# Optimization experiments

Hardware: AMD Instinct MI355X
Metric: run time of the kernel (lower is better)

Reference implementation:

```python
import jax, jax.numpy as jnp
import numpy as np

IN_FEATURES = 4096
OUT_FEATURES = 4096
CLUSTERING_FRAC = 0.1
IC = int(IN_FEATURES * CLUSTERING_FRAC)  # 409 clustering synapses
HILL_N = 2.0
HILL_KD = 0.5 ** 2  # k_a ** n
BATCH = 8192


def setup_inputs() -> dict:
    key = jax.random.key(0)
    k1, k2, k3, k4 = jax.random.split(key, 4)
    x = jax.random.normal(k1, (BATCH, IN_FEATURES), dtype=jnp.float32)
    # Linear default init scale ~ 1/sqrt(fan_in)
    W_nmda = jax.random.normal(k2, (OUT_FEATURES, IC), dtype=jnp.float32) / np.sqrt(IC)
    W_non = jax.random.normal(k3, (OUT_FEATURES, IN_FEATURES - IC), dtype=jnp.float32) / np.sqrt(IN_FEATURES - IC)
    b_non = jax.random.normal(k4, (OUT_FEATURES,), dtype=jnp.float32) / np.sqrt(IN_FEATURES - IC)
    return {"x": x, "W_nmda": W_nmda, "W_non": W_non, "b_non": b_non}


def reference(x, W_nmda, W_non, b_non):
    # Split synapses into clustering (nmda) and non-clustering groups.
    x_c = x[:, :IC]          # [B, 409]
    x_nc = x[:, IC:]         # [B, 3687]

    # state = sigmoid(non_nmda(x_nc)) - 1  (<= 0)
    state = jax.nn.sigmoid(x_nc @ W_non.T + b_non) - 1.0  # [B, O]

    # conv1d(kernel=[1,1], stride=1) over per-synapse products then sum over
    # window positions == weighted sum with coeff 2 for interior, 1 at edges.
    coeff = jnp.full((IC,), 2.0, dtype=x.dtype).at[0].set(1.0).at[-1].set(1.0)
    cluster_activity = (x_c * coeff) @ W_nmda.T  # [B, O]

    pre = cluster_activity + state
    # Hill(n=2, k_a=0.5): x^n / (k_d + x^n)
    xn = pre ** HILL_N
    return xn / (HILL_KD + xn)
```

## Files before the change

### kernel.cpp

```cpp
#include <hip/hip_runtime.h>
#include <hip/hip_bf16.h>
#include <cstdint>
#include <cstddef>

typedef unsigned short u16;
typedef __bf16 bf16x8 __attribute__((ext_vector_type(8)));
typedef float f32x4 __attribute__((ext_vector_type(4)));
typedef float f32x4u __attribute__((ext_vector_type(4), aligned(4)));

#define IN_F   4096
#define OUT_F  4096
#define IC_N   409
#define K_NON  3687
#define K_HI0  3712
#define K_LO0  4121
#define K_HI1  4530
#define K_END  4939
#define K_TOT  4992
#define BATCHN 8192
#define NT     78
#define T_SPLIT 58

__device__ __forceinline__ u16 f2bf(float f) {
  uint32_t u = __float_as_uint(f);
  uint32_t r = (u + 0x7FFFu + ((u >> 16) & 1u)) >> 16;
  return (u16)r;
}
__device__ __forceinline__ float bf2f(u16 h) {
  return __uint_as_float(((uint32_t)h) << 16);
}
__device__ __forceinline__ float coefj(int j) {
  return (j == 0 || j == IC_N - 1) ? 1.0f : 2.0f;
}

__global__ __launch_bounds__(256) void pack_a_kernel(const float* __restrict__ x,
                                                     u16* __restrict__ Ab) {
  __shared__ u16 hbuf[IC_N];
  __shared__ u16 lbuf[IC_N];
  const int row = blockIdx.x;
  const float* xr = x + (size_t)row * IN_F;
  for (int j = threadIdx.x; j < IC_N; j += 256) {
    const float v = xr[j] * coefj(j);
    const u16 h = f2bf(v);
    hbuf[j] = h;
    lbuf[j] = f2bf(v - bf2f(h));
  }
  __syncthreads();
  u16* outr = Ab + (size_t)row * K_TOT;
  for (int c8 = threadIdx.x; c8 < K_TOT / 8; c8 += 256) {
    const int kb = c8 * 8;
    u16 tmp[8] __attribute__((aligned(16)));
    if (kb + 8 <= K_NON) {
      const float* s = xr + IC_N + kb;
      const f32x4u v0 = *(const f32x4u*)s;
      const f32x4u v1 = *(const f32x4u*)(s + 4);
#pragma unroll
      for (int e = 0; e < 4; ++e) { tmp[e] = f2bf(v0[e]); tmp[4 + e] = f2bf(v1[e]); }
    } else if (kb < K_HI0) {
#pragma unroll
      for (int e = 0; e < 8; ++e) {
        const int k = kb + e;
        tmp[e] = (k < K_NON) ? f2bf(xr[IC_N + k]) : (u16)0;
      }
    } else {
#pragma unroll
      for (int e = 0; e < 8; ++e) {
        const int k = kb + e;
        u16 o;
        if (k < K_LO0)      o = hbuf[k - K_HI0];
        else if (k < K_HI1) o = lbuf[k - K_LO0];
        else if (k < K_END) o = hbuf[k - K_HI1];
        else                o = 0;
        tmp[e] = o;
      }
    }
    *(int4*)(outr + kb) = *(const int4*)tmp;
  }
}

__global__ __launch_bounds__(256) void pack_b_kernel(const float* __restrict__ Wnon,
                                                     const float* __restrict__ Wnmda,
                                                     u16* __restrict__ Bb) {
  __shared__ u16 hbuf[IC_N];
  __shared__ u16 lbuf[IC_N];
  const int row = blockIdx.x;
  const float* wr = Wnon + (size_t)row * K_NON;
  const float* wc = Wnmda + (size_t)row * IC_N;
  for (int j = threadIdx.x; j < IC_N; j += 256) {
    const float v = wc[j];
    const u16 h = f2bf(v);
    hbuf[j] = h;
    lbuf[j] = f2bf(v - bf2f(h));
  }
  __syncthreads();
  u16* outr = Bb + (size_t)row * K_TOT;
  for (int c8 = threadIdx.x; c8 < K_TOT / 8; c8 += 256) {
    const int kb = c8 * 8;
    u16 tmp[8] __attribute__((aligned(16)));
    if (kb + 8 <= K_NON) {
      const float* s = wr + kb;
      const f32x4u v0 = *(const f32x4u*)s;
      const f32x4u v1 = *(const f32x4u*)(s + 4);
#pragma unroll
      for (int e = 0; e < 4; ++e) { tmp[e] = f2bf(v0[e]); tmp[4 + e] = f2bf(v1[e]); }
    } else if (kb < K_HI0) {
#pragma unroll
      for (int e = 0; e < 8; ++e) {
        const int k = kb + e;
        tmp[e] = (k < K_NON) ? f2bf(wr[k]) : (u16)0;
      }
    } else {
#pragma unroll
      for (int e = 0; e < 8; ++e) {
        const int k = kb + e;
        u16 o;
        if (k < K_LO0)      o = hbuf[k - K_HI0];
        else if (k < K_HI1) o = hbuf[k - K_LO0];
        else if (k < K_END) o = lbuf[k - K_HI1];
        else                o = 0;
        tmp[e] = o;
      }
    }
    *(int4*)(outr + kb) = *(const int4*)tmp;
  }
}

#define GLOAD16(gp, lp)                                           \
  __builtin_amdgcn_global_load_lds(                               \
      (const __attribute__((address_space(1))) void*)(gp),        \
      (__attribute__((address_space(3))) void*)(lp), 16, 0, 0)

#define MEMFENCE() asm volatile("" ::: "memory")
#define BAR() do { MEMFENCE(); __builtin_amdgcn_s_barrier(); MEMFENCE(); } while (0)
#define LGKM0() asm volatile("s_waitcnt lgkmcnt(0)" ::: "memory")
#define VM6()   asm volatile("s_waitcnt vmcnt(6)" ::: "memory")
#define VM0()   asm volatile("s_waitcnt vmcnt(0)" ::: "memory")
#define VNONE   ((void)0)

#define RD_AF(SET, BW, KK, MH) do {                                    \
    _Pragma("unroll")                                                  \
    for (int mm = 0; mm < 4; ++mm)                                     \
      SET[mm] = *(const bf16x8*)(LDSc + (BW) * 65536 + (KK) * 16384 +  \
                 (wRow + (MH) * 64 + mm * 16) * 64 + laneOff);         \
  } while (0)
#define RD_BF(SET, BW, KK) do {                                        \
    _Pragma("unroll")                                                  \
    for (int n = 0; n < 4; ++n)                                        \
      SET[n] = *(const bf16x8*)(LDSc + (BW) * 65536 + 32768 +          \
                (KK) * 16384 + (wCol + n * 16) * 64 + laneOff);        \
  } while (0)

#define PHASE(AFC, BFC, MH, NEXT_READS, STAGE_STMT, VMSTMT) do {       \
    LGKM0();                                                           \
    NEXT_READS;                                                        \
    STAGE_STMT;                                                        \
    __builtin_amdgcn_sched_barrier(0);                                 \
    __builtin_amdgcn_s_setprio(1);                                     \
    _Pragma("unroll")                                                  \
    for (int mm = 0; mm < 4; ++mm)                                     \
      _Pragma("unroll")                                                \
      for (int n = 0; n < 4; ++n)                                      \
        acc[(MH) * 4 + mm][n] = __builtin_amdgcn_mfma_f32_16x16x32_bf16( \
            AFC[mm], BFC[n], acc[(MH) * 4 + mm][n], 0, 0, 0);          \
    __builtin_amdgcn_s_setprio(0);                                     \
    VMSTMT;                                                            \
    BAR();                                                             \
  } while (0)

__global__ __launch_bounds__(512, 1) void gemm_fused_kernel(
    const u16* __restrict__ Ab, const u16* __restrict__ Bb,
    const float* __restrict__ bnon, float* __restrict__ out) {
  __shared__ __attribute__((aligned(16))) u16 LDSu[65536];
  char* LDSc = (char*)LDSu;

  const int bid = blockIdx.x;
  const int swz = ((bid & 7) << 6) | (bid >> 3);
  const int bm = swz >> 4, bn = swz & 15;
  const int rowBase = bm * 256, colBase = bn * 256;

  const int tid  = threadIdx.x;
  const int w    = tid >> 6, lane = tid & 63;
  const int wm = w >> 2, wn = w & 3;
  const int wRow = wm * 128, wCol = wn * 64;
  const int l15 = lane & 15, g = lane >> 4;

  const int laneOff = ((l15 >> 1) << 7) +
                      (((((l15 & 1) << 2) | g) ^ ((l15 >> 1) & 7)) << 4);

  int rowS[2], colS[2];
#pragma unroll
  for (int is = 0; is < 2; ++is) {
    const int d = is * 8192 + tid * 16;
    const int b = d ^ ((d >> 3) & 0x70);
    rowS[is] = ((b >> 7) << 1) | ((b >> 6) & 1);
    colS[is] = (b >> 1) & 31;
  }
  const u16* pA0 = Ab + (size_t)(rowBase + rowS[0]) * K_TOT + colS[0];
  const u16* pA1 = Ab + (size_t)(rowBase + rowS[1]) * K_TOT + colS[1];
  const u16* pB0 = Bb + (size_t)(colBase + rowS[0]) * K_TOT + colS[0];
  const u16* pB1 = Bb + (size_t)(colBase + rowS[1]) * K_TOT + colS[1];

  float bn4[4];
#pragma unroll
  for (int n = 0; n < 4; ++n) bn4[n] = bnon[colBase + wCol + n * 16 + l15];
  asm volatile("" :: "v"(bn4[0]), "v"(bn4[1]), "v"(bn4[2]), "v"(bn4[3]));
  VM0();

  auto stageU = [&](int mat, int buf, int ks, int t64) {
    const u16* s0 = (mat ? pB0 : pA0) + t64 + ks * 32;
    const u16* s1 = (mat ? pB1 : pA1) + t64 + ks * 32;
    char* dst = LDSc + buf * 65536 + mat * 32768 + ks * 16384 + tid * 16;
    GLOAD16(s0, dst);
    GLOAD16(s1, dst + 8192);
  };

  f32x4 acc[8][4] = {};
  bf16x8 afA[4], afB[4], bfrA[4], bfrB[4];

  stageU(0, 0, 0, 0); stageU(1, 0, 0, 0);
  stageU(0, 0, 1, 0); stageU(1, 0, 1, 0);
  stageU(0, 1, 0, 64); stageU(1, 1, 0, 64);
  asm volatile("s_waitcnt vmcnt(8)" ::: "memory");
  BAR();
  RD_BF(bfrA, 0, 0); RD_AF(afA, 0, 0, 0);

  for (int T = 0; T < NT - 2; T += 2) {
    if (T == T_SPLIT) {
#pragma unroll
      for (int m = 0; m < 8; ++m)
#pragma unroll
        for (int n = 0; n < 4; ++n)
#pragma unroll
          for (int j = 0; j < 4; ++j) {
            const float t = acc[m][n][j] + bn4[n];
            acc[m][n][j] = 1.0f / (1.0f + __expf(-t)) - 1.0f;
          }
    }
    const int t1 = (T + 1) * 64, t2 = (T + 2) * 64, t3 = (T + 3) * 64;
    PHASE(afA, bfrA, 0, RD_AF(afB, 0, 0, 1),                           stageU(0, 1, 1, t1), VM6());
    PHASE(afB, bfrA, 1, { RD_BF(bfrB, 0, 1); RD_AF(afA, 0, 1, 0); },   stageU(1, 1, 1, t1), VNONE);
    PHASE(afA, bfrB, 0, RD_AF(afB, 0, 1, 1),                           stageU(0, 0, 0, t2), VM6());
    PHASE(afB, bfrB, 1, { RD_BF(bfrA, 1, 0); RD_AF(afA, 1, 0, 0); },   stageU(1, 0, 0, t2), VNONE);
    PHASE(afA, bfrA, 0, RD_AF(afB, 1, 0, 1),                           stageU(0, 0, 1, t2), VM6());
    PHASE(afB, bfrA, 1, { RD_BF(bfrB, 1, 1); RD_AF(afA, 1, 1, 0); },   stageU(1, 0, 1, t2), VNONE);
    PHASE(afA, bfrB, 0, RD_AF(afB, 1, 1, 1),                           stageU(0, 1, 0, t3), VM6());
    PHASE(afB, bfrB, 1, { RD_BF(bfrA, 0, 0); RD_AF(afA, 0, 0, 0); },   stageU(1, 1, 0, t3), VNONE);
  }

  {
    const int t1 = (NT - 1) * 64;
    PHASE(afA, bfrA, 0, RD_AF(afB, 0, 0, 1),                           stageU(0, 1, 1, t1), VM0());
    PHASE(afB, bfrA, 1, { RD_BF(bfrB, 0, 1); RD_AF(afA, 0, 1, 0); },   stageU(1, 1, 1, t1), VNONE);
    PHASE(afA, bfrB, 0, RD_AF(afB, 0, 1, 1),                           VNONE,               VM0());
    PHASE(afB, bfrB, 1, { RD_BF(bfrA, 1, 0); RD_AF(afA, 1, 0, 0); },   VNONE,               VNONE);
    PHASE(afA, bfrA, 0, RD_AF(afB, 1, 0, 1),                           VNONE,               VM0());
    PHASE(afB, bfrA, 1, { RD_BF(bfrB, 1, 1); RD_AF(afA, 1, 1, 0); },   VNONE,               VNONE);
    PHASE(afA, bfrB, 0, RD_AF(afB, 1, 1, 1),                           VNONE,               VM0());
    PHASE(afB, bfrB, 1, VNONE,                                         VNONE,               VNONE);
  }

#pragma unroll
  for (int m = 0; m < 8; ++m) {
#pragma unroll
    for (int n = 0; n < 4; ++n) {
#pragma unroll
      for (int j = 0; j < 4; ++j) {
        const int r = rowBase + wRow + m * 16 + g * 4 + j;
        const int c = colBase + wCol + n * 16 + l15;
        const float pre = acc[m][n][j];
        const float xn = pre * pre;
        out[(size_t)r * OUT_F + c] = xn / (0.25f + xn);
      }
    }
  }
}

__global__ void naive_fused_kernel(const float* __restrict__ x,
                                   const float* __restrict__ Wnmda,
                                   const float* __restrict__ Wnon,
                                   const float* __restrict__ bnon,
                                   float* __restrict__ out) {
  const long long total = (long long)BATCHN * OUT_F;
  for (long long idx = (long long)blockIdx.x * blockDim.x + threadIdx.x;
       idx < total; idx += (long long)gridDim.x * blockDim.x) {
    const int b = (int)(idx / OUT_F);
    const int o = (int)(idx % OUT_F);
    float s = bnon[o];
    for (int k = 0; k < K_NON; ++k)
      s += x[(size_t)b * IN_F + IC_N + k] * Wnon[(size_t)o * K_NON + k];
    const float state = 1.0f / (1.0f + __expf(-s)) - 1.0f;
    float ca = 0.0f;
    for (int j = 0; j < IC_N; ++j)
      ca += x[(size_t)b * IN_F + j] * coefj(j) * Wnmda[(size_t)o * IC_N + j];
    const float pre = ca + state;
    const float xn = pre * pre;
    out[idx] = xn / (0.25f + xn);
  }
}

extern "C" void kernel_launch(void* const* d_in, const int* in_sizes, int n_in,
                              void* d_out, int out_size, void* d_ws, size_t ws_size,
                              hipStream_t stream) {
  const float* x     = (const float*)d_in[0];
  const float* Wnmda = (const float*)d_in[1];
  const float* Wnon  = (const float*)d_in[2];
  const float* bnon  = (const float*)d_in[3];
  float* out = (float*)d_out;

  const size_t needA = (size_t)BATCHN * K_TOT * sizeof(u16);
  const size_t needB = (size_t)OUT_F * K_TOT * sizeof(u16);

  if (ws_size < needA + needB) {
    naive_fused_kernel<<<8192, 256, 0, stream>>>(x, Wnmda, Wnon, bnon, out);
    return;
  }

  u16* Ab = (u16*)d_ws;
  u16* Bb = Ab + (size_t)BATCHN * K_TOT;

  pack_a_kernel<<<BATCHN, 256, 0, stream>>>(x, Ab);
  pack_b_kernel<<<OUT_F, 256, 0, stream>>>(Wnon, Wnmda, Bb);
  gemm_fused_kernel<<<512, 512, 0, stream>>>(Ab, Bb, bnon, out);
}
```

Measured before the change: 358.7 us.

## Shrink GEMM block tile to 128x128 with four waves and two blocks per CU

Changes the fused GEMM from 256x256 tiles with 8 waves (512 blocks, one per CU) to 128x128 tiles with 4 waves (2048 blocks, two per CU). LDS use per block is halved, and the pipeline is simplified to four phases per iteration, each staging both A and B for a k-half. The aim is better load balance over 256 CUs and latency hiding across two resident blocks. In exchange, data reuse per tile drops, so global/L2 traffic per FLOP roughly doubles.

```diff
diff --git a/kernel.cpp b/kernel.cpp
--- a/kernel.cpp
+++ b/kernel.cpp
@@ -133,24 +133,24 @@
 #define MEMFENCE() asm volatile("" ::: "memory")
 #define BAR() do { MEMFENCE(); __builtin_amdgcn_s_barrier(); MEMFENCE(); } while (0)
 #define LGKM0() asm volatile("s_waitcnt lgkmcnt(0)" ::: "memory")
-#define VM6()   asm volatile("s_waitcnt vmcnt(6)" ::: "memory")
+#define VM8()   asm volatile("s_waitcnt vmcnt(8)" ::: "memory")
 #define VM0()   asm volatile("s_waitcnt vmcnt(0)" ::: "memory")
 #define VNONE   ((void)0)
 
-#define RD_AF(SET, BW, KK, MH) do {                                    \
+#define RD_AF(SET, BW, KK) do {                                        \
     _Pragma("unroll")                                                  \
     for (int mm = 0; mm < 4; ++mm)                                     \
-      SET[mm] = *(const bf16x8*)(LDSc + (BW) * 65536 + (KK) * 16384 +  \
-                 (wRow + (MH) * 64 + mm * 16) * 64 + laneOff);         \
+      SET[mm] = *(const bf16x8*)(LDSc + (BW) * 32768 + (KK) * 8192 +   \
+                 (wRow + mm * 16) * 64 + laneOff);                     \
   } while (0)
 #define RD_BF(SET, BW, KK) do {                                        \
     _Pragma("unroll")                                                  \
     for (int n = 0; n < 4; ++n)                                        \
-      SET[n] = *(const bf16x8*)(LDSc + (BW) * 65536 + 32768 +          \
-                (KK) * 16384 + (wCol + n * 16) * 64 + laneOff);        \
+      SET[n] = *(const bf16x8*)(LDSc + (BW) * 32768 + 16384 +          \
+                (KK) * 8192 + (wCol + n * 16) * 64 + laneOff);         \
   } while (0)
 
-#define PHASE(AFC, BFC, MH, NEXT_READS, STAGE_STMT, VMSTMT) do {       \
+#define PHASE(AFC, BFC, NEXT_READS, STAGE_STMT, VMSTMT) do {           \
     LGKM0();                                                           \
     NEXT_READS;                                                        \
     STAGE_STMT;                                                        \
@@ -160,28 +160,28 @@
     for (int mm = 0; mm < 4; ++mm)                                     \
       _Pragma("unroll")                                                \
       for (int n = 0; n < 4; ++n)                                      \
-        acc[(MH) * 4 + mm][n] = __builtin_amdgcn_mfma_f32_16x16x32_bf16( \
-            AFC[mm], BFC[n], acc[(MH) * 4 + mm][n], 0, 0, 0);          \
+        acc[mm][n] = __builtin_amdgcn_mfma_f32_16x16x32_bf16(          \
+            AFC[mm], BFC[n], acc[mm][n], 0, 0, 0);                     \
     __builtin_amdgcn_s_setprio(0);                                     \
     VMSTMT;                                                            \
     BAR();                                                             \
   } while (0)
 
-__global__ __launch_bounds__(512, 1) void gemm_fused_kernel(
+__global__ __launch_bounds__(256, 2) void gemm_fused_kernel(
     const u16* __restrict__ Ab, const u16* __restrict__ Bb,
     const float* __restrict__ bnon, float* __restrict__ out) {
-  __shared__ __attribute__((aligned(16))) u16 LDSu[65536];
+  __shared__ __attribute__((aligned(16))) u16 LDSu[32768];
   char* LDSc = (char*)LDSu;
 
   const int bid = blockIdx.x;
-  const int swz = ((bid & 7) << 6) | (bid >> 3);
-  const int bm = swz >> 4, bn = swz & 15;
-  const int rowBase = bm * 256, colBase = bn * 256;
+  const int swz = ((bid & 7) << 8) | (bid >> 3);
+  const int bm = swz >> 5, bn = swz & 31;
+  const int rowBase = bm * 128, colBase = bn * 128;
 
   const int tid  = threadIdx.x;
   const int w    = tid >> 6, lane = tid & 63;
-  const int wm = w >> 2, wn = w & 3;
-  const int wRow = wm * 128, wCol = wn * 64;
+  const int wm = w >> 1, wn = w & 1;
+  const int wRow = wm * 64, wCol = wn * 64;
   const int l15 = lane & 15, g = lane >> 4;
 
   const int laneOff = ((l15 >> 1) << 7) +
@@ -190,7 +190,7 @@
   int rowS[2], colS[2];
 #pragma unroll
   for (int is = 0; is < 2; ++is) {
-    const int d = is * 8192 + tid * 16;
+    const int d = is * 4096 + tid * 16;
     const int b = d ^ ((d >> 3) & 0x70);
     rowS[is] = ((b >> 7) << 1) | ((b >> 6) & 1);
     colS[is] = (b >> 1) & 31;
@@ -206,28 +206,31 @@
   asm volatile("" :: "v"(bn4[0]), "v"(bn4[1]), "v"(bn4[2]), "v"(bn4[3]));
   VM0();
 
-  auto stageU = [&](int mat, int buf, int ks, int t64) {
-    const u16* s0 = (mat ? pB0 : pA0) + t64 + ks * 32;
-    const u16* s1 = (mat ? pB1 : pA1) + t64 + ks * 32;
-    char* dst = LDSc + buf * 65536 + mat * 32768 + ks * 16384 + tid * 16;
+  auto stageS = [&](int mat, int buf, int kh, int t64) {
+    const u16* s0 = (mat ? pB0 : pA0) + t64 + kh * 32;
+    const u16* s1 = (mat ? pB1 : pA1) + t64 + kh * 32;
+    char* dst = LDSc + buf * 32768 + mat * 16384 + kh * 8192 + tid * 16;
     GLOAD16(s0, dst);
-    GLOAD16(s1, dst + 8192);
+    GLOAD16(s1, dst + 4096);
   };
-
-  f32x4 acc[8][4] = {};
+  auto stage2 = [&](int buf, int kh, int t64) {
+    stageS(0, buf, kh, t64);
+    stageS(1, buf, kh, t64);
+  };
+
+  f32x4 acc[4][4] = {};
   bf16x8 afA[4], afB[4], bfrA[4], bfrB[4];
 
-  stageU(0, 0, 0, 0); stageU(1, 0, 0, 0);
-  stageU(0, 0, 1, 0); stageU(1, 0, 1, 0);
-  stageU(0, 1, 0, 64); stageU(1, 1, 0, 64);
-  asm volatile("s_waitcnt vmcnt(8)" ::: "memory");
+  stage2(0, 0, 0);  stage2(0, 1, 0);
+  stage2(1, 0, 64); stage2(1, 1, 64);
+  VM8();
   BAR();
-  RD_BF(bfrA, 0, 0); RD_AF(afA, 0, 0, 0);
+  RD_AF(afA, 0, 0); RD_BF(bfrA, 0, 0);
 
   for (int T = 0; T < NT - 2; T += 2) {
     if (T == T_SPLIT) {
 #pragma unroll
-      for (int m = 0; m < 8; ++m)
+      for (int m = 0; m < 4; ++m)
 #pragma unroll
         for (int n = 0; n < 4; ++n)
 #pragma unroll
@@ -236,31 +239,22 @@
             acc[m][n][j] = 1.0f / (1.0f + __expf(-t)) - 1.0f;
           }
     }
-    const int t1 = (T + 1) * 64, t2 = (T + 2) * 64, t3 = (T + 3) * 64;
-    PHASE(afA, bfrA, 0, RD_AF(afB, 0, 0, 1),                           stageU(0, 1, 1, t1), VM6());
-    PHASE(afB, bfrA, 1, { RD_BF(bfrB, 0, 1); RD_AF(afA, 0, 1, 0); },   stageU(1, 1, 1, t1), VNONE);
-    PHASE(afA, bfrB, 0, RD_AF(afB, 0, 1, 1),                           stageU(0, 0, 0, t2), VM6());
-    PHASE(afB, bfrB, 1, { RD_BF(bfrA, 1, 0); RD_AF(afA, 1, 0, 0); },   stageU(1, 0, 0, t2), VNONE);
-    PHASE(afA, bfrA, 0, RD_AF(afB, 1, 0, 1),                           stageU(0, 0, 1, t2), VM6());
-    PHASE(afB, bfrA, 1, { RD_BF(bfrB, 1, 1); RD_AF(afA, 1, 1, 0); },   stageU(1, 0, 1, t2), VNONE);
-    PHASE(afA, bfrB, 0, RD_AF(afB, 1, 1, 1),                           stageU(0, 1, 0, t3), VM6());
-    PHASE(afB, bfrB, 1, { RD_BF(bfrA, 0, 0); RD_AF(afA, 0, 0, 0); },   stageU(1, 1, 0, t3), VNONE);
+    const int t2 = (T + 2) * 64, t3 = (T + 3) * 64;
+    PHASE(afA, bfrA, { RD_AF(afB, 0, 1); RD_BF(bfrB, 0, 1); }, stage2(0, 0, t2), VM8());
+    PHASE(afB, bfrB, { RD_AF(afA, 1, 0); RD_BF(bfrA, 1, 0); }, stage2(0, 1, t2), VM8());
+    PHASE(afA, bfrA, { RD_AF(afB, 1, 1); RD_BF(bfrB, 1, 1); }, stage2(1, 0, t3), VM8());
+    PHASE(afB, bfrB, { RD_AF(afA, 0, 0); RD_BF(bfrA, 0, 0); }, stage2(1, 1, t3), VM8());
   }
 
   {
-    const int t1 = (NT - 1) * 64;
-    PHASE(afA, bfrA, 0, RD_AF(afB, 0, 0, 1),                           stageU(0, 1, 1, t1), VM0());
-    PHASE(afB, bfrA, 1, { RD_BF(bfrB, 0, 1); RD_AF(afA, 0, 1, 0); },   stageU(1, 1, 1, t1), VNONE);
-    PHASE(afA, bfrB, 0, RD_AF(afB, 0, 1, 1),                           VNONE,               VM0());
-    PHASE(afB, bfrB, 1, { RD_BF(bfrA, 1, 0); RD_AF(afA, 1, 0, 0); },   VNONE,               VNONE);
-    PHASE(afA, bfrA, 0, RD_AF(afB, 1, 0, 1),                           VNONE,               VM0());
-    PHASE(afB, bfrA, 1, { RD_BF(bfrB, 1, 1); RD_AF(afA, 1, 1, 0); },   VNONE,               VNONE);
-    PHASE(afA, bfrB, 0, RD_AF(afB, 1, 1, 1),                           VNONE,               VM0());
-    PHASE(afB, bfrB, 1, VNONE,                                         VNONE,               VNONE);
-  }
-
-#pragma unroll
-  for (int m = 0; m < 8; ++m) {
+    PHASE(afA, bfrA, { RD_AF(afB, 0, 1); RD_BF(bfrB, 0, 1); }, VNONE, VM0());
+    PHASE(afB, bfrB, { RD_AF(afA, 1, 0); RD_BF(bfrA, 1, 0); }, VNONE, VNONE);
+    PHASE(afA, bfrA, { RD_AF(afB, 1, 1); RD_BF(bfrB, 1, 1); }, VNONE, VNONE);
+    PHASE(afB, bfrB, VNONE,                                    VNONE, VNONE);
+  }
+
+#pragma unroll
+  for (int m = 0; m < 4; ++m) {
 #pragma unroll
     for (int n = 0; n < 4; ++n) {
 #pragma unroll
@@ -320,5 +314,5 @@
 
   pack_a_kernel<<<BATCHN, 256, 0, stream>>>(x, Ab);
   pack_b_kernel<<<OUT_F, 256, 0, stream>>>(Wnon, Wnmda, Bb);
-  gemm_fused_kernel<<<512, 512, 0, stream>>>(Ab, Bb, bnon, out);
-}
+  gemm_fused_kernel<<<2048, 256, 0, stream>>>(Ab, Bb, bnon, out);
+}
```

Result: slower. 510.8 us (+42.4%).
